# Kernel tuning notes

Measured on AMD Instinct MI355X. Metric: run time of the kernel, lower is better.

Reference implementation:

```python
import jax, jax.numpy as jnp
import numpy as np

GROUPS = 32
N_HEADS = 8
EPS = 1e-5


def setup_inputs() -> dict:
    key = jax.random.key(0)
    ks = jax.random.split(key, 4)
    B, C, H, W = 8, 512, 32, 32
    x = jax.random.normal(ks[0], (B, C, H, W), dtype=jnp.float32)
    norm_scale = jnp.ones((C,), jnp.float32)
    norm_bias = jnp.zeros((C,), jnp.float32)
    qkv_w = jax.random.normal(ks[1], (3 * C, C), jnp.float32) * (C ** -0.5)
    qkv_b = jnp.zeros((3 * C,), jnp.float32)
    proj_w = jax.random.normal(ks[2], (C, C), jnp.float32) * (C ** -0.5)
    proj_b = jnp.zeros((C,), jnp.float32)
    return {"x": x, "norm_scale": norm_scale, "norm_bias": norm_bias,
            "qkv_w": qkv_w, "qkv_b": qkv_b, "proj_w": proj_w, "proj_b": proj_b}


def reference(x, norm_scale, norm_bias, qkv_w, qkv_b, proj_w, proj_b):
    B, C, H, W = x.shape
    T = H * W
    xf = x.reshape(B, C, T)

    # GroupNorm32 (32 groups, computed in float32, affine)
    xg = xf.astype(jnp.float32).reshape(B, GROUPS, C // GROUPS, T)
    mean = xg.mean(axis=(2, 3), keepdims=True)
    var = xg.var(axis=(2, 3), keepdims=True)
    xn = ((xg - mean) * jax.lax.rsqrt(var + EPS)).reshape(B, C, T)
    xn = (xn * norm_scale[:, None] + norm_bias[:, None]).astype(x.dtype)

    # qkv: 1x1 conv1d == pointwise matmul -> [B, 3C, T]
    qkv = jnp.einsum('oc,bct->bot', qkv_w, xn) + qkv_b[:, None]

    # QKVAttentionLegacy: reshape to [B*H, 3*ch, T], split
    ch = C // N_HEADS
    qkv_h = qkv.reshape(B * N_HEADS, 3 * ch, T)
    q, k, v = qkv_h[:, :ch], qkv_h[:, ch:2 * ch], qkv_h[:, 2 * ch:]
    scale = ch ** -0.25
    weight = jnp.einsum('bct,bcs->bts', q * scale, k * scale)  # [B*H, T, T]
    weight = jax.nn.softmax(weight.astype(jnp.float32), axis=-1).astype(qkv.dtype)
    a = jnp.einsum('bts,bcs->bct', weight, v).reshape(B, C, T)

    # proj_out (1x1 conv) + residual
    h = jnp.einsum('oc,bct->bot', proj_w, a) + proj_b[:, None]
    return (xf + h).reshape(B, C, H, W)
```

## Files before the change

kernel.cpp:

```cpp
#include <hip/hip_runtime.h>
#include <hip/hip_bf16.h>
#include <stdint.h>

typedef unsigned short u16;
typedef unsigned int u32;
typedef __bf16 bf16x8 __attribute__((ext_vector_type(8)));
typedef float f32x4 __attribute__((ext_vector_type(4)));


static __device__ __forceinline__ u16 f2bf(float f) {
  union { __hip_bfloat16 h; u16 u; } c;
  c.h = __float2bfloat16(f);
  return c.u;
}

static __device__ __forceinline__ u16 f2bf_t(float f) {
  union { float f; u32 u; } c;
  c.f = f;
  return (u16)(c.u >> 16);
}

static __device__ __forceinline__ void gload_lds16(const void* g, void* l) {
  __builtin_amdgcn_global_load_lds(
      (__attribute__((address_space(1))) u32*)(uintptr_t)g,
      (__attribute__((address_space(3))) u32*)l, 16, 0, 0);
}

__global__ __launch_bounds__(256) void prep(const float* __restrict__ wq,
                                            const float* __restrict__ wp,
                                            const float* __restrict__ x,
                                            u16* __restrict__ wqb,
                                            u16* __restrict__ wpb,
                                            float* __restrict__ st) {
  int blk = blockIdx.x;
  if (blk >= 256) {
    int idx = ((blk - 256) * 256 + threadIdx.x) * 4;
    const float* s;
    u16* d;
    if (idx < 786432) { s = wq + idx; d = wqb + idx; }
    else { int k = idx - 786432; s = wp + k; d = wpb + k; }
    float4 v = *(const float4*)s;
    uint2 o;
    o.x = (u32)f2bf(v.x) | ((u32)f2bf(v.y) << 16);
    o.y = (u32)f2bf(v.z) | ((u32)f2bf(v.w) << 16);
    *(uint2*)d = o;
    return;
  }
  int bg = blk;
  const float* p = x + (size_t)bg * 16384;
  float s1 = 0.f, s2 = 0.f;
  for (int i = threadIdx.x * 4; i < 16384; i += 1024) {
    float4 v = *(const float4*)(p + i);
    s1 += v.x + v.y + v.z + v.w;
    s2 += v.x * v.x + v.y * v.y + v.z * v.z + v.w * v.w;
  }
#pragma unroll
  for (int off = 1; off < 64; off <<= 1) {
    s1 += __shfl_xor(s1, off);
    s2 += __shfl_xor(s2, off);
  }
  __shared__ float r1[4], r2[4];
  int w = threadIdx.x >> 6, l = threadIdx.x & 63;
  if (l == 0) { r1[w] = s1; r2[w] = s2; }
  __syncthreads();
  if (threadIdx.x == 0) {
    float t1 = r1[0] + r1[1] + r1[2] + r1[3];
    float t2 = r2[0] + r2[1] + r2[2] + r2[3];
    float mean = t1 * (1.f / 16384.f);
    float var = t2 * (1.f / 16384.f) - mean * mean;
    st[bg * 2] = mean;
    st[bg * 2 + 1] = rsqrtf(var + 1e-5f);
  }
}

__global__ __launch_bounds__(256) void gn_apply(const float* __restrict__ x,
                                                const float* __restrict__ st,
                                                const float* __restrict__ ns,
                                                const float* __restrict__ nbi,
                                                u16* __restrict__ xnt) {
  __shared__ u16 tile[32 * 520];
  int b = blockIdx.x >> 5;
  int t0 = (blockIdx.x & 31) << 5;
  int tid = threadIdx.x;
  int tg = (tid & 7) * 4;
  int c0 = tid >> 3;
#pragma unroll 4
  for (int cc = 0; cc < 16; ++cc) {
    int c = cc * 32 + c0;
    float mean = st[(b * 32 + (c >> 4)) * 2];
    float rstd = st[(b * 32 + (c >> 4)) * 2 + 1];
    float sc = ns[c], bi = nbi[c];
    float4 v = *(const float4*)(x + (size_t)b * 524288 + (size_t)c * 1024 + t0 + tg);
    tile[(tg + 0) * 520 + c] = f2bf((v.x - mean) * rstd * sc + bi);
    tile[(tg + 1) * 520 + c] = f2bf((v.y - mean) * rstd * sc + bi);
    tile[(tg + 2) * 520 + c] = f2bf((v.z - mean) * rstd * sc + bi);
    tile[(tg + 3) * 520 + c] = f2bf((v.w - mean) * rstd * sc + bi);
  }
  __syncthreads();
#pragma unroll
  for (int i = 0; i < 8; ++i) {
    int chunk = i * 256 + tid;
    int tl2 = chunk >> 6;
    int c0b = (chunk & 63) * 8;
    uint4 d = *(const uint4*)(tile + tl2 * 520 + c0b);
    *(uint4*)(xnt + (size_t)b * 524288 + (size_t)(t0 + tl2) * 512 + c0b) = d;
  }
}

static __device__ __forceinline__ void gemm_core(const u16* Abase, const u16* Bbase,
                                                 f32x4 acc[4][4], u16* As, u16* Bs,
                                                 int w, int l, int wm, int wn) {
  const int r8 = l >> 3, ch = l & 7;
  const int fr = l & 15, fq = l >> 4;
#pragma unroll 1
  for (int kt = 0; kt < 8; ++kt) {
    __syncthreads();
#pragma unroll
    for (int i = 0; i < 4; ++i) {
      int gi = (w << 2) + i;
      int row = (gi << 3) + r8;
      int xoff = ((ch ^ (row & 7)) << 4);
      gload_lds16((const char*)Abase + (size_t)row * 1024 + (kt << 7) + xoff,
                  (char*)As + (gi << 10));
      gload_lds16((const char*)Bbase + (size_t)row * 1024 + (kt << 7) + xoff,
                  (char*)Bs + (gi << 10));
    }
    __syncthreads();
#pragma unroll
    for (int kf = 0; kf < 2; ++kf) {
      bf16x8 af[4], bfv[4];
#pragma unroll
      for (int i = 0; i < 4; ++i) {
        int rowA = wm * 64 + i * 16 + fr;
        af[i] = *(const bf16x8*)(As + rowA * 64 + ((((kf << 2) + fq) ^ (rowA & 7)) << 3));
        int rowB = wn * 64 + i * 16 + fr;
        bfv[i] = *(const bf16x8*)(Bs + rowB * 64 + ((((kf << 2) + fq) ^ (rowB & 7)) << 3));
      }
#pragma unroll
      for (int i = 0; i < 4; ++i)
#pragma unroll
        for (int j = 0; j < 4; ++j)
          acc[i][j] = __builtin_amdgcn_mfma_f32_16x16x32_bf16(af[i], bfv[j], acc[i][j], 0, 0, 0);
    }
  }
}

__global__ __launch_bounds__(256) void gemm_qkv(const u16* __restrict__ Wq,
                                                const u16* __restrict__ Xnt,
                                                const float* __restrict__ bq,
                                                u16* __restrict__ qT,
                                                u16* __restrict__ kT,
                                                u16* __restrict__ vv) {
  __shared__ u16 SMEM[18432];
  int bid0 = blockIdx.x;
  int bid = (bid0 & 7) * 96 + (bid0 >> 3);
  int mb = bid % 12, nb = (bid / 12) % 8, b = bid / 96;
  int tid = threadIdx.x, w = tid >> 6, l = tid & 63;
  int wm = tid >> 7, wn = (tid >> 6) & 1;
  int fr = l & 15, fq = l >> 4;
  f32x4 acc[4][4];
#pragma unroll
  for (int i = 0; i < 4; ++i)
#pragma unroll
    for (int j = 0; j < 4; ++j) acc[i][j] = (f32x4){0.f, 0.f, 0.f, 0.f};

  gemm_core(Wq + (size_t)mb * 65536, Xnt + (size_t)b * 524288 + (size_t)nb * 65536,
            acc, SMEM, SMEM + 8192, w, l, wm, wn);

  __syncthreads();

  int seg2 = mb * 2 + wm;
  int h = seg2 / 3, typ = seg2 % 3;
  size_t hb = (size_t)(b * 8 + h) * 65536;
  u16* SUB = SMEM + wm * 9216;

  if (typ < 2) {
    float qksc = (typ == 0) ? 0.51011687f : 0.35355339f;
#pragma unroll
    for (int i = 0; i < 4; ++i) {
      int oi = i * 16 + fq * 4;
      float4 bb = *(const float4*)(bq + mb * 128 + wm * 64 + oi);
#pragma unroll
      for (int j = 0; j < 4; ++j) {
        int tl = wn * 64 + j * 16 + fr;
        f32x4 v = acc[i][j];
        uint2 pk;
        pk.x = (u32)f2bf((v[0] + bb.x) * qksc) | ((u32)f2bf((v[1] + bb.y) * qksc) << 16);
        pk.y = (u32)f2bf((v[2] + bb.z) * qksc) | ((u32)f2bf((v[3] + bb.w) * qksc) << 16);
        *(uint2*)(SUB + tl * 72 + oi) = pk;
      }
    }
  } else {
#pragma unroll
    for (int i = 0; i < 4; ++i) {
      int oi = i * 16 + fq * 4;
      float4 bb = *(const float4*)(bq + mb * 128 + wm * 64 + oi);
      float bbv[4] = {bb.x, bb.y, bb.z, bb.w};
#pragma unroll
      for (int j = 0; j < 4; ++j) {
        int tl = wn * 64 + j * 16 + fr;
        f32x4 v = acc[i][j];
#pragma unroll
        for (int r = 0; r < 4; ++r)
          SUB[(oi + r) * 136 + tl] = f2bf(v[r] + bbv[r]);
      }
    }
  }
  __syncthreads();

  int lt = tid & 127;
  if (typ < 2) {
    u16* dstb = (typ == 0 ? qT : kT) + hb;
#pragma unroll
    for (int it = 0; it < 8; ++it) {
      int slot = it * 128 + lt;
      int t = slot >> 3, chk = slot & 7;
      uint4 val = *(const uint4*)(SUB + t * 72 + chk * 8);
      *(uint4*)(dstb + (size_t)(nb * 128 + t) * 64 + chk * 8) = val;
    }
  } else {
#pragma unroll
    for (int it = 0; it < 8; ++it) {
      int slot = it * 128 + lt;
      int c = slot >> 4, chk = slot & 15;
      uint4 val = *(const uint4*)(SUB + c * 136 + chk * 8);
      *(uint4*)(vv + hb + (size_t)c * 1024 + nb * 128 + chk * 8) = val;
    }
  }
}

__global__ __launch_bounds__(512) void attn(const u16* __restrict__ qT,
                                            const u16* __restrict__ kT,
                                            const u16* __restrict__ vv,
                                            u16* __restrict__ aT) {
  __shared__ u16 Ks[128 * 64];
  __shared__ u16 Vs[64 * 128];
  __shared__ u16 Ps[8 * 16 * 72];
  int bid = blockIdx.x;
  int bh = (bid & 7) * 8 + (bid >> 6);
  int tq = (bid >> 3) & 7;
  int tid = threadIdx.x, w = tid >> 6, l = tid & 63;
  int fr = l & 15, fq = l >> 4;
  int r8 = l >> 3, ch = l & 7;
  size_t hb = (size_t)bh * 65536;

  bf16x8 aq[2];
  {
    const u16* qp = qT + hb + (size_t)(tq * 128 + w * 16 + fr) * 64 + fq * 8;
    aq[0] = *(const bf16x8*)(qp);
    aq[1] = *(const bf16x8*)(qp + 32);
  }

  union { u32 u[4]; bf16x8 v; } onesu;
#pragma unroll
  for (int i = 0; i < 4; ++i) onesu.u[i] = 0x3F803F80u;
  const bf16x8 vone = onesu.v;

  f32x4 acc_o[4];
  f32x4 acc_s = (f32x4){0.f, 0.f, 0.f, 0.f};
#pragma unroll
  for (int nb = 0; nb < 4; ++nb) acc_o[nb] = (f32x4){0.f, 0.f, 0.f, 0.f};

  u16* pw = Ps + w * (16 * 72);

#pragma unroll 1
  for (int st = 0; st < 8; ++st) {
    __syncthreads();
#pragma unroll
    for (int j = 0; j < 2; ++j) {
      int gi = w * 2 + j;
      int row = gi * 8 + r8;
      int xoff = ((ch ^ (row & 7)) << 4);
      gload_lds16((const char*)(kT + hb) + (size_t)(st * 128 + row) * 128 + xoff,
                  (char*)Ks + (gi << 10));
      int c = gi * 4 + (l >> 4);
      int half = (l >> 3) & 1;
      int ch8 = l & 7;
      int sxoff = half * 128 + ((ch8 ^ (c & 7)) << 4);
      gload_lds16((const char*)(vv + hb) + (size_t)c * 2048 + st * 256 + sxoff,
                  (char*)Vs + (gi << 10));
    }
    __syncthreads();

#pragma unroll
    for (int sh = 0; sh < 2; ++sh) {
      f32x4 sa[4];
#pragma unroll
      for (int nb = 0; nb < 4; ++nb) sa[nb] = (f32x4){0.f, 0.f, 0.f, 0.f};
      __builtin_amdgcn_s_setprio(1);
#pragma unroll
      for (int nb = 0; nb < 4; ++nb) {
        int krow = sh * 64 + nb * 16 + fr;
#pragma unroll
        for (int kf = 0; kf < 2; ++kf) {
          bf16x8 bk = *(const bf16x8*)(Ks + krow * 64 + ((((kf << 2) + fq) ^ (krow & 7)) << 3));
          sa[nb] = __builtin_amdgcn_mfma_f32_16x16x32_bf16(aq[kf], bk, sa[nb], 0, 0, 0);
        }
      }
      __builtin_amdgcn_s_setprio(0);

#pragma unroll
      for (int nb = 0; nb < 4; ++nb)
#pragma unroll
        for (int r = 0; r < 4; ++r)
          pw[(fq * 4 + r) * 72 + nb * 16 + fr] = f2bf_t(exp2f(sa[nb][r]));

      bf16x8 ap[2];
#pragma unroll
      for (int kf = 0; kf < 2; ++kf)
        ap[kf] = *(const bf16x8*)(pw + fr * 72 + kf * 32 + fq * 8);

      __builtin_amdgcn_s_setprio(1);
#pragma unroll
      for (int nb = 0; nb < 4; ++nb) {
        int vrow = nb * 16 + fr;
#pragma unroll
        for (int kf = 0; kf < 2; ++kf) {
          bf16x8 bv = *(const bf16x8*)(Vs + vrow * 128 + sh * 64 +
                                       ((((kf << 2) + fq) ^ (vrow & 7)) << 3));
          acc_o[nb] = __builtin_amdgcn_mfma_f32_16x16x32_bf16(ap[kf], bv, acc_o[nb], 0, 0, 0);
        }
      }
#pragma unroll
      for (int kf = 0; kf < 2; ++kf)
        acc_s = __builtin_amdgcn_mfma_f32_16x16x32_bf16(ap[kf], vone, acc_s, 0, 0, 0);
      __builtin_amdgcn_s_setprio(0);
    }
  }

  int b = bh >> 3, h = bh & 7;
  f32x4 invl;
#pragma unroll
  for (int r = 0; r < 4; ++r) invl[r] = 1.f / acc_s[r];
#pragma unroll
  for (int nb = 0; nb < 4; ++nb) {
    f32x4 ov = acc_o[nb] * invl;
#pragma unroll
    for (int r = 0; r < 4; ++r) {
      int t = tq * 128 + w * 16 + fq * 4 + r;
      aT[(size_t)b * 524288 + (size_t)t * 512 + h * 64 + nb * 16 + fr] = f2bf(ov[r]);
    }
  }
}

__global__ __launch_bounds__(256) void gemm_proj(const u16* __restrict__ Wp,
                                                 const u16* __restrict__ aT,
                                                 const float* __restrict__ bp,
                                                 const float* __restrict__ x,
                                                 float* __restrict__ out) {
  __shared__ u16 As[128 * 64];
  __shared__ u16 Bs[128 * 64];
  int bid0 = blockIdx.x;
  int bid = (bid0 & 7) * 32 + (bid0 >> 3);
  int mb = bid & 3, nb = (bid >> 2) & 7, b = bid >> 5;
  int tid = threadIdx.x, w = tid >> 6, l = tid & 63;
  int wm = w >> 1, wn = w & 1;
  f32x4 acc[4][4];
#pragma unroll
  for (int i = 0; i < 4; ++i)
#pragma unroll
    for (int j = 0; j < 4; ++j) acc[i][j] = (f32x4){0.f, 0.f, 0.f, 0.f};

  gemm_core(Wp + (size_t)mb * 65536, aT + (size_t)b * 524288 + (size_t)nb * 65536,
            acc, As, Bs, w, l, wm, wn);

  int fr = l & 15, fq = l >> 4;
#pragma unroll
  for (int i = 0; i < 4; ++i) {
    int o0 = mb * 128 + wm * 64 + i * 16 + fq * 4;
    float b0 = bp[o0], b1 = bp[o0 + 1], b2 = bp[o0 + 2], b3 = bp[o0 + 3];
#pragma unroll
    for (int j = 0; j < 4; ++j) {
      int t = nb * 128 + wn * 64 + j * 16 + fr;
      f32x4 v = acc[i][j];
      size_t base = (size_t)b * 524288 + (size_t)o0 * 1024 + t;
      out[base] = x[base] + v[0] + b0;
      out[base + 1024] = x[base + 1024] + v[1] + b1;
      out[base + 2048] = x[base + 2048] + v[2] + b2;
      out[base + 3072] = x[base + 3072] + v[3] + b3;
    }
  }
}

extern "C" void kernel_launch(void* const* d_in, const int* in_sizes, int n_in,
                              void* d_out, int out_size, void* d_ws, size_t ws_size,
                              hipStream_t stream) {
  const float* x = (const float*)d_in[0];
  const float* ns = (const float*)d_in[1];
  const float* nbi = (const float*)d_in[2];
  const float* wq = (const float*)d_in[3];
  const float* bq = (const float*)d_in[4];
  const float* wp = (const float*)d_in[5];
  const float* bp = (const float*)d_in[6];
  float* out = (float*)d_out;
  char* ws = (char*)d_ws;

  u16* wqb = (u16*)(ws);
  u16* wpb = (u16*)(ws + 1572864);
  float* st = (float*)(ws + 2097152);
  u16* xnt = (u16*)(ws + 2101248);
  u16* qT = (u16*)(ws + 2101248 + 8388608);
  u16* kT = (u16*)(ws + 2101248 + 2 * 8388608);
  u16* vv = (u16*)(ws + 2101248 + 3 * 8388608);
  u16* aT = xnt;

  hipLaunchKernelGGL(prep, dim3(1280), dim3(256), 0, stream, wq, wp, x, wqb, wpb, st);
  hipLaunchKernelGGL(gn_apply, dim3(256), dim3(256), 0, stream, x, st, ns, nbi, xnt);
  hipLaunchKernelGGL(gemm_qkv, dim3(768), dim3(256), 0, stream, wqb, xnt, bq, qT, kT, vv);
  hipLaunchKernelGGL(attn, dim3(512), dim3(512), 0, stream, qT, kT, vv, aT);
  hipLaunchKernelGGL(gemm_proj, dim3(256), dim3(256), 0, stream, wpb, aT, bp, x, out);
}
```

Baseline: 87.75 us.

## Prefetch next K/V tile into registers while computing current tile

Replaces the direct global-to-LDS loads at the top of each attention tile iteration with register prefetching: the next K/V tile is loaded into registers before the MFMA work on the current tile, then written to LDS between two barriers. The aim is to hide global memory latency behind compute instead of stalling on the load at each step. It costs extra VGPRs for the staging registers and replaces the async LDS-load path with ordinary loads and stores.

```diff
diff --git a/kernel.cpp b/kernel.cpp
--- a/kernel.cpp
+++ b/kernel.cpp
@@ -251,6 +251,25 @@
     aq[1] = *(const bf16x8*)(qp + 32);
   }
 
+  const char* ksrc[2];
+  const char* vsrc[2];
+  char* kdst[2];
+  char* vdst[2];
+#pragma unroll
+  for (int j = 0; j < 2; ++j) {
+    int gi = w * 2 + j;
+    int row = gi * 8 + r8;
+    int xoff = ((ch ^ (row & 7)) << 4);
+    ksrc[j] = (const char*)(kT + hb) + (size_t)row * 128 + xoff;
+    kdst[j] = (char*)Ks + (gi << 10) + l * 16;
+    int c = gi * 4 + (l >> 4);
+    int half = (l >> 3) & 1;
+    int ch8 = l & 7;
+    int sxoff = half * 128 + ((ch8 ^ (c & 7)) << 4);
+    vsrc[j] = (const char*)(vv + hb) + (size_t)c * 2048 + sxoff;
+    vdst[j] = (char*)Vs + (gi << 10) + l * 16;
+  }
+
   union { u32 u[4]; bf16x8 v; } onesu;
 #pragma unroll
   for (int i = 0; i < 4; ++i) onesu.u[i] = 0x3F803F80u;
@@ -263,24 +282,28 @@
 
   u16* pw = Ps + w * (16 * 72);
 
+  {
+    uint4 kr0 = *(const uint4*)(ksrc[0]);
+    uint4 kr1 = *(const uint4*)(ksrc[1]);
+    uint4 vr0 = *(const uint4*)(vsrc[0]);
+    uint4 vr1 = *(const uint4*)(vsrc[1]);
+    *(uint4*)(kdst[0]) = kr0;
+    *(uint4*)(kdst[1]) = kr1;
+    *(uint4*)(vdst[0]) = vr0;
+    *(uint4*)(vdst[1]) = vr1;
+  }
+  __syncthreads();
+
 #pragma unroll 1
   for (int st = 0; st < 8; ++st) {
-    __syncthreads();
-#pragma unroll
-    for (int j = 0; j < 2; ++j) {
-      int gi = w * 2 + j;
-      int row = gi * 8 + r8;
-      int xoff = ((ch ^ (row & 7)) << 4);
-      gload_lds16((const char*)(kT + hb) + (size_t)(st * 128 + row) * 128 + xoff,
-                  (char*)Ks + (gi << 10));
-      int c = gi * 4 + (l >> 4);
-      int half = (l >> 3) & 1;
-      int ch8 = l & 7;
-      int sxoff = half * 128 + ((ch8 ^ (c & 7)) << 4);
-      gload_lds16((const char*)(vv + hb) + (size_t)c * 2048 + st * 256 + sxoff,
-                  (char*)Vs + (gi << 10));
-    }
-    __syncthreads();
+    uint4 kreg[2], vreg[2];
+    if (st < 7) {
+#pragma unroll
+      for (int j = 0; j < 2; ++j) {
+        kreg[j] = *(const uint4*)(ksrc[j] + (size_t)(st + 1) * 16384);
+        vreg[j] = *(const uint4*)(vsrc[j] + (size_t)(st + 1) * 256);
+      }
+    }
 
 #pragma unroll
     for (int sh = 0; sh < 2; ++sh) {
@@ -325,6 +348,16 @@
       for (int kf = 0; kf < 2; ++kf)
         acc_s = __builtin_amdgcn_mfma_f32_16x16x32_bf16(ap[kf], vone, acc_s, 0, 0, 0);
       __builtin_amdgcn_s_setprio(0);
+    }
+
+    if (st < 7) {
+      __syncthreads();
+#pragma unroll
+      for (int j = 0; j < 2; ++j) {
+        *(uint4*)(kdst[j]) = kreg[j];
+        *(uint4*)(vdst[j]) = vreg[j];
+      }
+      __syncthreads();
     }
   }
 
```

Result: slower. 103.3 us (+17.8%).

## Double-buffer K/V tiles in attention and vectorize P stores via transposed S

Applied to the files above, without the earlier changes.

The attention kernel now loads 64-key K/V tiles into two alternating LDS buffers, prefetching the next tile while computing on the current one, with a single barrier per iteration instead of two. The QK^T MFMA operands are swapped so each lane holds consecutive key columns, which lets the exp'd probabilities be packed and written to LDS as 8-byte stores instead of scalar 2-byte stores. The cost is twice as many loop iterations, with the same total LDS footprint for K/V. Prefetch overlap relies on the async global-to-LDS loads completing before the end-of-iteration barrier.

```diff
diff --git a/kernel.cpp b/kernel.cpp
--- a/kernel.cpp
+++ b/kernel.cpp
@@ -233,8 +233,8 @@
                                             const u16* __restrict__ kT,
                                             const u16* __restrict__ vv,
                                             u16* __restrict__ aT) {
-  __shared__ u16 Ks[128 * 64];
-  __shared__ u16 Vs[64 * 128];
+  __shared__ u16 Ks[2][64 * 64];
+  __shared__ u16 Vs[2][64 * 64];
   __shared__ u16 Ps[8 * 16 * 72];
   int bid = blockIdx.x;
   int bh = (bid & 7) * 8 + (bid >> 6);
@@ -263,69 +263,73 @@
 
   u16* pw = Ps + w * (16 * 72);
 
+  int srow = w * 8 + r8;
+  int sxoff = ((ch ^ (srow & 7)) << 4);
+  const char* ksrc = (const char*)(kT + hb) + (size_t)srow * 128 + sxoff;
+  const char* vsrc = (const char*)(vv + hb) + (size_t)srow * 2048 + sxoff;
+
+#define ATTN_STAGE(buf, stt)                                         \
+  {                                                                  \
+    gload_lds16(ksrc + (size_t)(stt) * 8192, (char*)Ks[buf] + (w << 10)); \
+    gload_lds16(vsrc + (size_t)(stt) * 128, (char*)Vs[buf] + (w << 10));  \
+  }
+
+  ATTN_STAGE(0, 0);
+  __syncthreads();
+
 #pragma unroll 1
-  for (int st = 0; st < 8; ++st) {
+  for (int st = 0; st < 16; ++st) {
+    int cur = st & 1;
+    if (st < 15) ATTN_STAGE(cur ^ 1, st + 1);
+    const u16* Kb = Ks[cur];
+    const u16* Vb = Vs[cur];
+
+    f32x4 sa[4];
+#pragma unroll
+    for (int nb = 0; nb < 4; ++nb) sa[nb] = (f32x4){0.f, 0.f, 0.f, 0.f};
+    __builtin_amdgcn_s_setprio(1);
+#pragma unroll
+    for (int nb = 0; nb < 4; ++nb) {
+      int krow = nb * 16 + fr;
+#pragma unroll
+      for (int kf = 0; kf < 2; ++kf) {
+        bf16x8 bk = *(const bf16x8*)(Kb + krow * 64 + ((((kf << 2) + fq) ^ (krow & 7)) << 3));
+        sa[nb] = __builtin_amdgcn_mfma_f32_16x16x32_bf16(bk, aq[kf], sa[nb], 0, 0, 0);
+      }
+    }
+    __builtin_amdgcn_s_setprio(0);
+
+#pragma unroll
+    for (int nb = 0; nb < 4; ++nb) {
+      float p0 = exp2f(sa[nb][0]), p1 = exp2f(sa[nb][1]);
+      float p2 = exp2f(sa[nb][2]), p3 = exp2f(sa[nb][3]);
+      uint2 pk;
+      pk.x = (u32)f2bf_t(p0) | ((u32)f2bf_t(p1) << 16);
+      pk.y = (u32)f2bf_t(p2) | ((u32)f2bf_t(p3) << 16);
+      *(uint2*)(pw + fr * 72 + nb * 16 + fq * 4) = pk;
+    }
+
+    bf16x8 ap[2];
+#pragma unroll
+    for (int kf = 0; kf < 2; ++kf)
+      ap[kf] = *(const bf16x8*)(pw + fr * 72 + kf * 32 + fq * 8);
+
+    __builtin_amdgcn_s_setprio(1);
+#pragma unroll
+    for (int nb = 0; nb < 4; ++nb) {
+      int vrow = nb * 16 + fr;
+#pragma unroll
+      for (int kf = 0; kf < 2; ++kf) {
+        bf16x8 bv = *(const bf16x8*)(Vb + vrow * 64 + ((((kf << 2) + fq) ^ (vrow & 7)) << 3));
+        acc_o[nb] = __builtin_amdgcn_mfma_f32_16x16x32_bf16(ap[kf], bv, acc_o[nb], 0, 0, 0);
+      }
+    }
+#pragma unroll
+    for (int kf = 0; kf < 2; ++kf)
+      acc_s = __builtin_amdgcn_mfma_f32_16x16x32_bf16(ap[kf], vone, acc_s, 0, 0, 0);
+    __builtin_amdgcn_s_setprio(0);
+
     __syncthreads();
-#pragma unroll
-    for (int j = 0; j < 2; ++j) {
-      int gi = w * 2 + j;
-      int row = gi * 8 + r8;
-      int xoff = ((ch ^ (row & 7)) << 4);
-      gload_lds16((const char*)(kT + hb) + (size_t)(st * 128 + row) * 128 + xoff,
-                  (char*)Ks + (gi << 10));
-      int c = gi * 4 + (l >> 4);
-      int half = (l >> 3) & 1;
-      int ch8 = l & 7;
-      int sxoff = half * 128 + ((ch8 ^ (c & 7)) << 4);
-      gload_lds16((const char*)(vv + hb) + (size_t)c * 2048 + st * 256 + sxoff,
-                  (char*)Vs + (gi << 10));
-    }
-    __syncthreads();
-
-#pragma unroll
-    for (int sh = 0; sh < 2; ++sh) {
-      f32x4 sa[4];
-#pragma unroll
-      for (int nb = 0; nb < 4; ++nb) sa[nb] = (f32x4){0.f, 0.f, 0.f, 0.f};
-      __builtin_amdgcn_s_setprio(1);
-#pragma unroll
-      for (int nb = 0; nb < 4; ++nb) {
-        int krow = sh * 64 + nb * 16 + fr;
-#pragma unroll
-        for (int kf = 0; kf < 2; ++kf) {
-          bf16x8 bk = *(const bf16x8*)(Ks + krow * 64 + ((((kf << 2) + fq) ^ (krow & 7)) << 3));
-          sa[nb] = __builtin_amdgcn_mfma_f32_16x16x32_bf16(aq[kf], bk, sa[nb], 0, 0, 0);
-        }
-      }
-      __builtin_amdgcn_s_setprio(0);
-
-#pragma unroll
-      for (int nb = 0; nb < 4; ++nb)
-#pragma unroll
-        for (int r = 0; r < 4; ++r)
-          pw[(fq * 4 + r) * 72 + nb * 16 + fr] = f2bf_t(exp2f(sa[nb][r]));
-
-      bf16x8 ap[2];
-#pragma unroll
-      for (int kf = 0; kf < 2; ++kf)
-        ap[kf] = *(const bf16x8*)(pw + fr * 72 + kf * 32 + fq * 8);
-
-      __builtin_amdgcn_s_setprio(1);
-#pragma unroll
-      for (int nb = 0; nb < 4; ++nb) {
-        int vrow = nb * 16 + fr;
-#pragma unroll
-        for (int kf = 0; kf < 2; ++kf) {
-          bf16x8 bv = *(const bf16x8*)(Vs + vrow * 128 + sh * 64 +
-                                       ((((kf << 2) + fq) ^ (vrow & 7)) << 3));
-          acc_o[nb] = __builtin_amdgcn_mfma_f32_16x16x32_bf16(ap[kf], bv, acc_o[nb], 0, 0, 0);
-        }
-      }
-#pragma unroll
-      for (int kf = 0; kf < 2; ++kf)
-        acc_s = __builtin_amdgcn_mfma_f32_16x16x32_bf16(ap[kf], vone, acc_s, 0, 0, 0);
-      __builtin_amdgcn_s_setprio(0);
-    }
   }
 
   int b = bh >> 3, h = bh & 7;
@@ -341,6 +345,7 @@
       aT[(size_t)b * 524288 + (size_t)t * 512 + h * 64 + nb * 16 + fr] = f2bf(ov[r]);
     }
   }
+#undef ATTN_STAGE
 }
 
 __global__ __launch_bounds__(256) void gemm_proj(const u16* __restrict__ Wp,
```

Result: slower. 89.82 us (+2.4%).
